# Kernel optimization log

Hardware: AMD Instinct MI355X
Metric: run time of the kernel (lower is better)

The kernel has to match this reference:

```python
import jax, jax.numpy as jnp
import numpy as np

# ---- constants from the module ----
E_L, E_e, E_i = -65.0, 0.0, -80.0
V_th, V_reset, V_floor = -50.0, -65.0, -200.0
dt = 0.25
T_STEPS = 4000
DECAY_AMPA = float(np.exp(-dt / 2.0))   # tau_ampa = 2.0
DECAY_GABA = float(np.exp(-dt / 9.0))   # tau_gaba = 9.0
C_M_E, G_L_E = 1.0, 1.0 / 20.0          # tau_m_E = 20
C_M_I, G_L_I = 0.5, 0.5 / 5.0           # tau_m_I = 5
REF_E = 12                               # round(3.0/0.25)
REF_I = 6                                # round(1.5/0.25)
CM_BACK = 80.0
SLOPE = 1.0                              # biophysical surrogate slope

@jax.custom_vjp
def spike(u):
    # Heaviside forward, fast-sigmoid surrogate backward (SurrogateSpike)
    return (u >= 0).astype(u.dtype)

def _spike_fwd(u):
    return (u >= 0).astype(u.dtype), u

def _spike_bwd(u, g):
    return (g * SLOPE / (1.0 + SLOPE * jnp.abs(u)) ** 2,)

spike.defvjp(_spike_fwd, _spike_bwd)

def _scale_grad(x, scale):
    # forward identity, gradient scaled by `scale`
    return x * scale + jax.lax.stop_gradient(x) * (1.0 - scale)

def lif_step(v, I_total, ref, C_m, g_L, ref_steps):
    dv = (dt / C_m) * (-g_L * (v - E_L) + I_total)
    dv = _scale_grad(dv, 1.0 / CM_BACK)
    v = jnp.maximum(v + dv, V_floor)
    ref = jnp.maximum(ref - 1, 0)
    can_spike = ref == 0
    s = spike(v - V_th) * can_spike.astype(v.dtype)
    spiked_or_ref = (s > 0) | ~can_spike
    v = jnp.where(spiked_or_ref, V_reset, v)
    ref = jnp.where(s > 0, ref_steps, ref)
    return v, s, ref

def setup_inputs() -> dict:
    key = jax.random.key(0)
    ks = jax.random.split(key, 6)
    T, B, N_IN, N_E, N_I, N_OUT = T_STEPS, 64, 64, 256, 64, 10

    def init_w(k, shape, mean, std):
        # init_weight: N(mean,std) clamped >=0, fan-in normalized
        w = jnp.maximum(jax.random.normal(k, shape, jnp.float32) * std + mean, 0.0)
        return w / shape[0]

    return {
        "input_spikes": (jax.random.uniform(ks[0], (T, B, N_IN)) < 0.02).astype(jnp.float32),
        "W_ff0": init_w(ks[1], (N_IN, N_E), 5.1, 3.8),
        "W_ff1": init_w(ks[2], (N_E, N_OUT), 5.1, 3.8),
        "W_ee": init_w(ks[3], (N_E, N_E), 0.0, 0.0),
        "W_ei": init_w(ks[4], (N_E, N_I), 1.0, 0.5),
        "W_ie": init_w(ks[5], (N_I, N_E), 3.0, 1.5),
    }

def reference(input_spikes, W_ff0, W_ff1, W_ee, W_ei, W_ie):
    # Dale's law: feedforward weights clamped >= 0 in forward
    W0 = jnp.maximum(W_ff0, 0.0)
    W1 = jnp.maximum(W_ff1, 0.0)
    B = input_spikes.shape[1]
    N_E, N_I, N_OUT = W0.shape[1], W_ei.shape[1], W1.shape[1]
    f32 = input_spikes.dtype

    z = lambda n: jnp.zeros((B, n), f32)
    vl = lambda n: jnp.full((B, n), E_L, f32)
    zr = lambda n: jnp.zeros((B, n), jnp.int32)

    carry0 = (vl(N_E), zr(N_E), z(N_E), z(N_E), z(N_E),   # E pop: v, ref, g_ampa, g_gaba, spikes
              vl(N_I), zr(N_I), z(N_I), z(N_I),           # I pop: v, ref, g_ampa, spikes
              vl(N_OUT), zr(N_OUT), z(N_OUT),             # out pop: v, ref, g_ampa
              z(N_OUT))                                    # output spike accumulator

    def step(c, s_in):
        v_e, r_e, ge_e, gi_e, s_e, v_i, r_i, ge_i, s_i, v_o, r_o, g_o, acc = c
        # exp_synapse: spike kicks first, then decay
        ge_e = (ge_e + s_in @ W0 + s_e @ W_ee) * DECAY_AMPA
        gi_e = (gi_e + s_i @ W_ie) * DECAY_GABA
        ge_i = (ge_i + s_e @ W_ei) * DECAY_AMPA
        # E neurons: COBA with excitation + inhibition
        v_e, s_e, r_e = lif_step(v_e, ge_e * (E_e - v_e) + gi_e * (E_i - v_e), r_e, C_M_E, G_L_E, REF_E)
        # I neurons: COBA excitation only
        v_i, s_i, r_i = lif_step(v_i, ge_i * (E_e - v_i), r_i, C_M_I, G_L_I, REF_I)
        # output layer driven by fresh E spikes
        g_o = (g_o + s_e @ W1) * DECAY_AMPA
        v_o, s_o, r_o = lif_step(v_o, g_o * (E_e - v_o), r_o, C_M_E, G_L_E, REF_E)
        acc = acc + s_o
        return (v_e, r_e, ge_e, gi_e, s_e, v_i, r_i, ge_i, s_i, v_o, r_o, g_o, acc), None

    cT, _ = jax.lax.scan(step, carry0, input_spikes)
    return cT[-1]  # [B, N_OUT] output spike counts over T_steps
```

## Files before the change

### kernel.cpp

```cpp
#include <hip/hip_runtime.h>
#include <math.h>

#pragma clang fp contract(off)

#define BB 64
#define N_IN 64
#define N_E 256
#define N_I 64
#define N_OUT 10

__device__ inline unsigned long long rfl64(unsigned long long x) {
  unsigned int lo = __builtin_amdgcn_readfirstlane((unsigned int)x);
  unsigned int hi = __builtin_amdgcn_readfirstlane((unsigned int)(x >> 32));
  return (((unsigned long long)hi) << 32) | (unsigned long long)lo;
}

__global__ __launch_bounds__(320, 1) void ping_kernel(
    const float* __restrict__ g_in,
    const float* __restrict__ g_W0,
    const float* __restrict__ g_W1,
    const float* __restrict__ g_Wee,
    const float* __restrict__ g_Wei,
    const float* __restrict__ g_Wie,
    float* __restrict__ g_out,
    int T, float dA, float dG)
{
  const int tid  = threadIdx.x;
  const int lane = tid & 63;
  const int wav  = tid >> 6;
  const int b    = blockIdx.x;
  const int col  = (lane < N_OUT) ? lane : 0;
  const int colO = 64 + col;
  const int base64 = wav * 64;

  __shared__ float sWie[N_I * N_E];
  __shared__ float sWeiO[N_E * 80];
  __shared__ float sZeroRow[256];
  __shared__ __align__(16) float sPK[2][64][4];
  __shared__ __align__(16) float sKoT[2][16][4];
  __shared__ __align__(16) unsigned sTag[2][4];
  __shared__ __align__(8) unsigned long long sMI[2];
  __shared__ unsigned sMITag[2];
  __shared__ unsigned long long sME[2][4];
  __shared__ int sWee;

  {
    const float4* s0 = (const float4*)g_Wie; float4* d0 = (float4*)sWie;
    for (int k = tid; k < (N_I * N_E) / 4; k += 320) d0[k] = s0[k];
    const float4* wei4 = (const float4*)g_Wei;
    for (int k = tid; k < 256 * 16; k += 320) {
      int r = k >> 4, c4 = k & 15;
      *(float4*)&sWeiO[r * 80 + c4 * 4] = wei4[k];
    }
    for (int k = tid; k < 256 * N_OUT; k += 320) {
      int r = k / N_OUT, o = k - r * N_OUT;
      sWeiO[r * 80 + 64 + o] = fmaxf(g_W1[k], 0.f);
    }
    for (int k = tid; k < 256 * 6; k += 320) {
      int r = k / 6, c = k - r * 6;
      sWeiO[r * 80 + 74 + c] = 0.f;
    }
    for (int k = tid; k < 256; k += 320) sZeroRow[k] = 0.f;
  }
  if (tid < 8) sTag[tid >> 2][tid & 3] = 0u;
  if (tid < 8) sME[tid >> 2][tid & 3] = 0ull;
  if (tid < 2) { sMI[tid] = 0ull; sMITag[tid] = 0u; }
  if (tid == 0) sWee = 0;
  __syncthreads();
  {
    bool any = false;
    const float4* p = (const float4*)g_Wee;
    for (int k = tid; k < (N_E * N_E) / 4; k += 320) {
      float4 x = p[k];
      any |= (x.x != 0.f) | (x.y != 0.f) | (x.z != 0.f) | (x.w != 0.f);
    }
    if (any) sWee = 1;
  }
  __syncthreads();
  const int wee = sWee;

  float vE = -65.f, ge = 0.f, gi = 0.f; int rE = 0;
  unsigned long long mE = 0ull;
  float vI = -65.f, gI = 0.f; int rI = 0;
  unsigned long long mI = 0ull;
  float vO = -65.f, gO = 0.f, accO = 0.f; int rO = 0;

  float cur = 0.f, n1 = 0.f;
  unsigned long long mInC = 0ull, aRemC = 0ull;
  bool vaC[4] = {false, false, false, false};
  float fwC[4];
  if (wav < 4) {
    cur = g_in[b * N_IN + lane];
    n1  = g_in[((T > 1 ? 1 : 0) * BB + b) * N_IN + lane];
    mInC = __ballot(cur != 0.f);
    if (mInC) {
      unsigned long long a = mInC;
      int ja[4];
#pragma unroll
      for (int k = 0; k < 4; ++k) {
        vaC[k] = (a != 0ull); ja[k] = vaC[k] ? (__ffsll(a) - 1) : 0; a &= (a - 1ull);
      }
      aRemC = a;
#pragma unroll
      for (int k = 0; k < 4; ++k) fwC[k] = g_W0[ja[k] * N_E + tid];
    }
  }

  if (wav < 4) {
    if (!wee) {
      for (int t = 0; t < T; ++t) {
        const int slot = t & 1;
        const int slotP = (t + 1) & 1;
        unsigned tgP = *((volatile unsigned*)&sMITag[slotP]);
        unsigned long long mdP = *((volatile unsigned long long*)&sMI[slotP]);

        const int tp = (t + 2 < T) ? (t + 2) : (T - 1);
        float n2 = g_in[(tp * BB + b) * N_IN + lane];

        float pEI = 0.f, kow = 0.f;
        {
          unsigned long long e = mE;
          while (e) {
            const float* qb[8];
#pragma unroll
            for (int k = 0; k < 8; ++k) {
              bool v = (e != 0ull); int j = v ? (__ffsll(e) - 1) : 0; e &= (e - 1ull);
              qb[k] = v ? &sWeiO[(base64 + j) * 80] : sZeroRow;
            }
            float fq[8], fr[8];
#pragma unroll
            for (int k = 0; k < 8; ++k) { fq[k] = qb[k][lane]; fr[k] = qb[k][colO]; }
#pragma unroll
            for (int k = 0; k < 8; ++k) pEI += fq[k];
#pragma unroll
            for (int k = 0; k < 8; ++k) kow += fr[k];
          }
        }

        sPK[slot][lane][wav] = pEI;
        if (lane < 16) sKoT[slot][lane][wav] = kow;
        asm volatile("" ::: "memory");
        if (lane == 0) *((volatile unsigned*)&sTag[slot][wav]) = (unsigned)(t + 1);

        unsigned long long mIc;
        if (tgP == (unsigned)t) {
          mIc = mdP;
        } else {
          volatile unsigned* vt = (volatile unsigned*)&sMITag[slotP];
          while (*vt != (unsigned)t) {}
          asm volatile("" ::: "memory");
          mIc = *((volatile unsigned long long*)&sMI[slotP]);
        }

        float kie = 0.f;
        {
          unsigned long long c = mIc;
          while (c) {
            const float* pb[8];
#pragma unroll
            for (int k = 0; k < 8; ++k) {
              bool v = (c != 0ull); int j = v ? (__ffsll(c) - 1) : 0; c &= (c - 1ull);
              pb[k] = v ? &sWie[j * N_E] : sZeroRow;
            }
            float fI[8];
#pragma unroll
            for (int k = 0; k < 8; ++k) fI[k] = pb[k][tid];
#pragma unroll
            for (int k = 0; k < 8; ++k) kie += fI[k];
          }
        }

        float kin = 0.f;
        if (mInC) {
#pragma unroll
          for (int k = 0; k < 4; ++k) kin += vaC[k] ? fmaxf(fwC[k], 0.f) : 0.f;
          while (aRemC) {
            int j = __ffsll(aRemC) - 1; aRemC &= (aRemC - 1ull);
            kin += fmaxf(g_W0[j * N_E + tid], 0.f);
          }
        }

        ge = (ge + kin) * dA;
        gi = (gi + kie) * dG;
        {
          float t2 = ge * (0.f - vE);
          float t3 = gi * (-80.f - vE);
          float Itot = t2 + t3;
          float dv = 0.25f * ((-0.05f) * (vE - (-65.f)) + Itot);
          dv = dv * 0.0125f + dv * 0.9875f;
          vE = fmaxf(vE + dv, -200.f);
          rE = rE - 1; if (rE < 0) rE = 0;
          bool can = (rE == 0);
          bool sE = ((vE - (-50.f)) >= 0.f) && can;
          vE = (sE || !can) ? -65.f : vE;
          rE = sE ? 12 : rE;
          mE = __ballot(sE);
        }

        mInC = __ballot(n1 != 0.f);
        aRemC = 0ull;
        vaC[0] = vaC[1] = vaC[2] = vaC[3] = false;
        if (mInC) {
          unsigned long long a = mInC;
          int ja[4];
#pragma unroll
          for (int k = 0; k < 4; ++k) {
            vaC[k] = (a != 0ull); ja[k] = vaC[k] ? (__ffsll(a) - 1) : 0; a &= (a - 1ull);
          }
          aRemC = a;
#pragma unroll
          for (int k = 0; k < 4; ++k) fwC[k] = g_W0[ja[k] * N_E + tid];
        }

        cur = n1; n1 = n2;
      }
    } else {
      unsigned long long we0 = 0ull, we1 = 0ull, we2 = 0ull, we3 = 0ull;
      for (int t = 0; t < T; ++t) {
        const int slot = t & 1;
        const int tp = (t + 2 < T) ? (t + 2) : (T - 1);
        float n2 = g_in[(tp * BB + b) * N_IN + lane];

        float pEI = 0.f, kow = 0.f;
        {
          unsigned long long e = mE;
          while (e) {
            const float* qb[4];
#pragma unroll
            for (int k = 0; k < 4; ++k) {
              bool v = (e != 0ull); int j = v ? (__ffsll(e) - 1) : 0; e &= (e - 1ull);
              qb[k] = v ? &sWeiO[(base64 + j) * 80] : sZeroRow;
            }
            float fq[4], fr[4];
#pragma unroll
            for (int k = 0; k < 4; ++k) { fq[k] = qb[k][lane]; fr[k] = qb[k][colO]; }
#pragma unroll
            for (int k = 0; k < 4; ++k) pEI += fq[k];
#pragma unroll
            for (int k = 0; k < 4; ++k) kow += fr[k];
          }
        }
        sPK[slot][lane][wav] = pEI;
        if (lane < 16) sKoT[slot][lane][wav] = kow;
        asm volatile("s_waitcnt lgkmcnt(0)" ::: "memory");
        if (lane == 0) *((volatile unsigned*)&sTag[slot][wav]) = (unsigned)(t + 1);

        float kie = 0.f;
        {
          unsigned long long c = mI;
          while (c) {
            const float* pb[8];
#pragma unroll
            for (int k = 0; k < 8; ++k) {
              bool v = (c != 0ull); int j = v ? (__ffsll(c) - 1) : 0; c &= (c - 1ull);
              pb[k] = v ? &sWie[j * N_E] : sZeroRow;
            }
            float fI[8];
#pragma unroll
            for (int k = 0; k < 8; ++k) fI[k] = pb[k][tid];
#pragma unroll
            for (int k = 0; k < 8; ++k) kie += fI[k];
          }
        }

        float kin = 0.f;
        if (mInC) {
#pragma unroll
          for (int k = 0; k < 4; ++k) kin += vaC[k] ? fmaxf(fwC[k], 0.f) : 0.f;
          while (aRemC) {
            int j = __ffsll(aRemC) - 1; aRemC &= (aRemC - 1ull);
            kin += fmaxf(g_W0[j * N_E + tid], 0.f);
          }
        }

        float kee = 0.f;
        {
          unsigned long long m0 = we0, m1 = we1, m2 = we2, m3 = we3;
          while (m0 | m1 | m2 | m3) {
            int idx = 0;
            if (m0)      { idx = __ffsll(m0) - 1;       m0 &= (m0 - 1ull); }
            else if (m1) { idx = 64 + __ffsll(m1) - 1;  m1 &= (m1 - 1ull); }
            else if (m2) { idx = 128 + __ffsll(m2) - 1; m2 &= (m2 - 1ull); }
            else         { idx = 192 + __ffsll(m3) - 1; m3 &= (m3 - 1ull); }
            kee += g_Wee[idx * N_E + tid];
          }
        }

        ge = ((ge + kin) + kee) * dA;
        gi = (gi + kie) * dG;
        {
          float t2 = ge * (0.f - vE);
          float t3 = gi * (-80.f - vE);
          float Itot = t2 + t3;
          float dv = 0.25f * ((-0.05f) * (vE - (-65.f)) + Itot);
          dv = dv * 0.0125f + dv * 0.9875f;
          vE = fmaxf(vE + dv, -200.f);
          rE = rE - 1; if (rE < 0) rE = 0;
          bool can = (rE == 0);
          bool sE = ((vE - (-50.f)) >= 0.f) && can;
          vE = (sE || !can) ? -65.f : vE;
          rE = sE ? 12 : rE;
          unsigned long long fresh = __ballot(sE);
          if (lane == 0) sME[slot][wav] = fresh;
          mE = fresh;
        }

        mInC = __ballot(n1 != 0.f);
        aRemC = 0ull;
        vaC[0] = vaC[1] = vaC[2] = vaC[3] = false;
        if (mInC) {
          unsigned long long a = mInC;
          int ja[4];
#pragma unroll
          for (int k = 0; k < 4; ++k) {
            vaC[k] = (a != 0ull); ja[k] = vaC[k] ? (__ffsll(a) - 1) : 0; a &= (a - 1ull);
          }
          aRemC = a;
#pragma unroll
          for (int k = 0; k < 4; ++k) fwC[k] = g_W0[ja[k] * N_E + tid];
        }

        {
          const unsigned want = (unsigned)(t + 1);
          const unsigned long long want2 = (((unsigned long long)want) << 32) | want;
          volatile unsigned long long* vt = (volatile unsigned long long*)&sTag[slot][0];
          while (true) {
            unsigned long long a0 = vt[0], a1 = vt[1];
            if (((a0 ^ want2) | (a1 ^ want2)) == 0ull) break;
          }
          asm volatile("" ::: "memory");
        }

        float4 P = *(const float4*)&sPK[slot][lane][0];
        float4 K = *(const float4*)&sKoT[slot][col][0];

        {
          float p = ((P.x + P.y) + P.z) + P.w;
          gI = (gI + p) * dA;
          float Ii = gI * (0.f - vI);
          float dvi = 0.5f * ((-0.1f) * (vI - (-65.f)) + Ii);
          dvi = dvi * 0.0125f + dvi * 0.9875f;
          vI = fmaxf(vI + dvi, -200.f);
          rI = rI - 1; if (rI < 0) rI = 0;
          bool canI = (rI == 0);
          bool sI = ((vI - (-50.f)) >= 0.f) && canI;
          vI = (sI || !canI) ? -65.f : vI;
          rI = sI ? 6 : rI;
          mI = __ballot(sI);
        }

        {
          float ko = ((K.x + K.y) + K.z) + K.w;
          gO = (gO + ko) * dA;
          float Io = gO * (0.f - vO);
          float dvo = 0.25f * ((-0.05f) * (vO - (-65.f)) + Io);
          dvo = dvo * 0.0125f + dvo * 0.9875f;
          vO = fmaxf(vO + dvo, -200.f);
          rO = rO - 1; if (rO < 0) rO = 0;
          bool canO = (rO == 0);
          bool sO = ((vO - (-50.f)) >= 0.f) && canO;
          vO = (sO || !canO) ? -65.f : vO;
          rO = sO ? 12 : rO;
          accO += sO ? 1.f : 0.f;
        }

        __syncthreads();
        we0 = rfl64(sME[slot][0]); we1 = rfl64(sME[slot][1]);
        we2 = rfl64(sME[slot][2]); we3 = rfl64(sME[slot][3]);

        cur = n1; n1 = n2;
      }
    }
  } else {
    if (!wee) {
      for (int t = 0; t < T; ++t) {
        const int slot = t & 1;
        {
          const unsigned want = (unsigned)(t + 1);
          const unsigned long long want2 = (((unsigned long long)want) << 32) | want;
          volatile unsigned long long* vt = (volatile unsigned long long*)&sTag[slot][0];
          while (true) {
            unsigned long long a0 = vt[0], a1 = vt[1];
            if (((a0 ^ want2) | (a1 ^ want2)) == 0ull) break;
          }
          asm volatile("" ::: "memory");
        }
        float4 P = *(const float4*)&sPK[slot][lane][0];
        float4 K = *(const float4*)&sKoT[slot][col][0];

        unsigned long long mIv;
        {
          float p = ((P.x + P.y) + P.z) + P.w;
          gI = (gI + p) * dA;
          float Ii = gI * (0.f - vI);
          float dvi = 0.5f * ((-0.1f) * (vI - (-65.f)) + Ii);
          dvi = dvi * 0.0125f + dvi * 0.9875f;
          vI = fmaxf(vI + dvi, -200.f);
          rI = rI - 1; if (rI < 0) rI = 0;
          bool canI = (rI == 0);
          bool sI = ((vI - (-50.f)) >= 0.f) && canI;
          vI = (sI || !canI) ? -65.f : vI;
          rI = sI ? 6 : rI;
          mIv = __ballot(sI);
        }

        {
          float ko = ((K.x + K.y) + K.z) + K.w;
          gO = (gO + ko) * dA;
          float Io = gO * (0.f - vO);
          float dvo = 0.25f * ((-0.05f) * (vO - (-65.f)) + Io);
          dvo = dvo * 0.0125f + dvo * 0.9875f;
          vO = fmaxf(vO + dvo, -200.f);
          rO = rO - 1; if (rO < 0) rO = 0;
          bool canO = (rO == 0);
          bool sO = ((vO - (-50.f)) >= 0.f) && canO;
          vO = (sO || !canO) ? -65.f : vO;
          rO = sO ? 12 : rO;
          accO += sO ? 1.f : 0.f;
        }

        if (lane == 0) {
          sMI[slot] = mIv;
          asm volatile("" ::: "memory");
          *((volatile unsigned*)&sMITag[slot]) = (unsigned)(t + 1);
        }
      }
    } else {
      for (int t = 0; t < T; ++t) __syncthreads();
    }
  }

  if (!wee) {
    float kd = 0.f;
    if (wav < 4) {
      unsigned long long e = mE;
      while (e) {
        const float* rb[8];
#pragma unroll
        for (int k = 0; k < 8; ++k) {
          bool v = (e != 0ull); int j = v ? (__ffsll(e) - 1) : 0; e &= (e - 1ull);
          rb[k] = v ? &sWeiO[(base64 + j) * 80] : sZeroRow;
        }
        float fr[8];
#pragma unroll
        for (int k = 0; k < 8; ++k) fr[k] = rb[k][colO];
#pragma unroll
        for (int k = 0; k < 8; ++k) kd += fr[k];
      }
    }
    __syncthreads();
    if (wav < 4 && lane < 16) sKoT[0][lane][wav] = kd;
    __syncthreads();
    if (wav == 4) {
      float4 K = *(const float4*)&sKoT[0][col][0];
      float ko = ((K.x + K.y) + K.z) + K.w;
      gO = (gO + ko) * dA;
      float Io = gO * (0.f - vO);
      float dvo = 0.25f * ((-0.05f) * (vO - (-65.f)) + Io);
      dvo = dvo * 0.0125f + dvo * 0.9875f;
      vO = fmaxf(vO + dvo, -200.f);
      rO = rO - 1; if (rO < 0) rO = 0;
      bool canO = (rO == 0);
      bool sO = ((vO - (-50.f)) >= 0.f) && canO;
      accO += sO ? 1.f : 0.f;
      if (lane < N_OUT) g_out[b * N_OUT + lane] = accO;
    }
  } else {
    float kd = 0.f;
    if (wav < 4) {
      unsigned long long e = mE;
      while (e) {
        const float* rb[4];
#pragma unroll
        for (int k = 0; k < 4; ++k) {
          bool v = (e != 0ull); int j = v ? (__ffsll(e) - 1) : 0; e &= (e - 1ull);
          rb[k] = v ? &sWeiO[(base64 + j) * 80] : sZeroRow;
        }
        float fr[4];
#pragma unroll
        for (int k = 0; k < 4; ++k) fr[k] = rb[k][colO];
#pragma unroll
        for (int k = 0; k < 4; ++k) kd += fr[k];
      }
    }
    __syncthreads();
    if (wav < 4 && lane < 16) sKoT[0][lane][wav] = kd;
    __syncthreads();
    if (wav < 4) {
      float4 K = *(const float4*)&sKoT[0][col][0];
      float ko = ((K.x + K.y) + K.z) + K.w;
      gO = (gO + ko) * dA;
      float Io = gO * (0.f - vO);
      float dvo = 0.25f * ((-0.05f) * (vO - (-65.f)) + Io);
      dvo = dvo * 0.0125f + dvo * 0.9875f;
      vO = fmaxf(vO + dvo, -200.f);
      rO = rO - 1; if (rO < 0) rO = 0;
      bool canO = (rO == 0);
      bool sO = ((vO - (-50.f)) >= 0.f) && canO;
      accO += sO ? 1.f : 0.f;
      if (wav == 0 && lane < N_OUT) g_out[b * N_OUT + lane] = accO;
    }
  }
}

extern "C" void kernel_launch(void* const* d_in, const int* in_sizes, int n_in,
                              void* d_out, int out_size, void* d_ws, size_t ws_size,
                              hipStream_t stream) {
  const float* g_in  = (const float*)d_in[0];
  const float* g_W0  = (const float*)d_in[1];
  const float* g_W1  = (const float*)d_in[2];
  const float* g_Wee = (const float*)d_in[3];
  const float* g_Wei = (const float*)d_in[4];
  const float* g_Wie = (const float*)d_in[5];
  float* out = (float*)d_out;
  int T = in_sizes[0] / (BB * N_IN);
  float dA = (float)exp(-0.25 / 2.0);
  float dG = (float)exp(-0.25 / 9.0);
  ping_kernel<<<dim3(BB), dim3(320), 0, stream>>>(g_in, g_W0, g_W1, g_Wee, g_Wei, g_Wie, out, T, dA, dG);
}
```

Measured before the change: 4.745 ms.

## Software-pipeline spike-weight gathers across timesteps and publish I-spike mask earlier

```diff
diff --git a/kernel.cpp b/kernel.cpp
--- a/kernel.cpp
+++ b/kernel.cpp
@@ -108,18 +108,27 @@
 
   if (wav < 4) {
     if (!wee) {
+      float fqP[8], frP[8], fIP[8];
+      unsigned long long mERem = 0ull;
+      unsigned long long mKieRem = 0ull;
+      bool kieHave = false;
+
+#pragma unroll
+      for (int k = 0; k < 8; ++k) { fqP[k] = sZeroRow[lane]; frP[k] = sZeroRow[colO]; }
+
       for (int t = 0; t < T; ++t) {
         const int slot = t & 1;
-        const int slotP = (t + 1) & 1;
-        unsigned tgP = *((volatile unsigned*)&sMITag[slotP]);
-        unsigned long long mdP = *((volatile unsigned long long*)&sMI[slotP]);
 
         const int tp = (t + 2 < T) ? (t + 2) : (T - 1);
         float n2 = g_in[(tp * BB + b) * N_IN + lane];
 
         float pEI = 0.f, kow = 0.f;
-        {
-          unsigned long long e = mE;
+#pragma unroll
+        for (int k = 0; k < 8; ++k) pEI += fqP[k];
+#pragma unroll
+        for (int k = 0; k < 8; ++k) kow += frP[k];
+        {
+          unsigned long long e = mERem;
           while (e) {
             const float* qb[8];
 #pragma unroll
@@ -142,19 +151,11 @@
         asm volatile("" ::: "memory");
         if (lane == 0) *((volatile unsigned*)&sTag[slot][wav]) = (unsigned)(t + 1);
 
-        unsigned long long mIc;
-        if (tgP == (unsigned)t) {
-          mIc = mdP;
-        } else {
-          volatile unsigned* vt = (volatile unsigned*)&sMITag[slotP];
-          while (*vt != (unsigned)t) {}
-          asm volatile("" ::: "memory");
-          mIc = *((volatile unsigned long long*)&sMI[slotP]);
-        }
-
         float kie = 0.f;
-        {
-          unsigned long long c = mIc;
+        if (kieHave) {
+#pragma unroll
+          for (int k = 0; k < 8; ++k) kie += fIP[k];
+          unsigned long long c = mKieRem;
           while (c) {
             const float* pb[8];
 #pragma unroll
@@ -210,6 +211,40 @@
           aRemC = a;
 #pragma unroll
           for (int k = 0; k < 4; ++k) fwC[k] = g_W0[ja[k] * N_E + tid];
+        }
+
+        {
+          unsigned long long e = mE;
+#pragma unroll
+          for (int k = 0; k < 8; ++k) {
+            bool v = (e != 0ull); int j = v ? (__ffsll(e) - 1) : 0; e &= (e - 1ull);
+            const float* q = v ? &sWeiO[(base64 + j) * 80] : sZeroRow;
+            fqP[k] = q[lane]; frP[k] = q[colO];
+          }
+          mERem = e;
+        }
+
+        {
+          unsigned tg = *((volatile unsigned*)&sMITag[slot]);
+          unsigned long long md = *((volatile unsigned long long*)&sMI[slot]);
+          unsigned long long mIc;
+          if (tg == (unsigned)(t + 1)) {
+            mIc = md;
+          } else {
+            volatile unsigned* vt = (volatile unsigned*)&sMITag[slot];
+            while (*vt != (unsigned)(t + 1)) {}
+            asm volatile("" ::: "memory");
+            mIc = *((volatile unsigned long long*)&sMI[slot]);
+          }
+          kieHave = (mIc != 0ull);
+          unsigned long long c = mIc;
+#pragma unroll
+          for (int k = 0; k < 8; ++k) {
+            bool v = (c != 0ull); int j = v ? (__ffsll(c) - 1) : 0; c &= (c - 1ull);
+            const float* p = v ? &sWie[j * N_E] : sZeroRow;
+            fIP[k] = p[tid];
+          }
+          mKieRem = c;
         }
 
         cur = n1; n1 = n2;
@@ -388,7 +423,6 @@
         float4 P = *(const float4*)&sPK[slot][lane][0];
         float4 K = *(const float4*)&sKoT[slot][col][0];
 
-        unsigned long long mIv;
         {
           float p = ((P.x + P.y) + P.z) + P.w;
           gI = (gI + p) * dA;
@@ -401,7 +435,12 @@
           bool sI = ((vI - (-50.f)) >= 0.f) && canI;
           vI = (sI || !canI) ? -65.f : vI;
           rI = sI ? 6 : rI;
-          mIv = __ballot(sI);
+          unsigned long long mIv = __ballot(sI);
+          if (lane == 0) {
+            sMI[slot] = mIv;
+            asm volatile("" ::: "memory");
+            *((volatile unsigned*)&sMITag[slot]) = (unsigned)(t + 1);
+          }
         }
 
         {
@@ -417,12 +456,6 @@
           vO = (sO || !canO) ? -65.f : vO;
           rO = sO ? 12 : rO;
           accO += sO ? 1.f : 0.f;
-        }
-
-        if (lane == 0) {
-          sMI[slot] = mIv;
-          asm volatile("" ::: "memory");
-          *((volatile unsigned*)&sMITag[slot]) = (unsigned)(t + 1);
         }
       }
     } else {
```

Result: slower. 5.237 ms (+10.4%).
